# Kernel optimization log

Hardware: AMD Instinct MI355X
Metric: run time of the kernel (lower is better)

The kernel has to match this reference:

```python
import jax, jax.numpy as jnp
import numpy as np

NEG_SLOPE = 0.2  # PyG GATConv default
EPS = 1e-16      # PyG softmax denominator guard


def setup_inputs() -> dict:
    key = jax.random.key(0)
    k1, k2, k3, k4, k5 = jax.random.split(key, 5)
    N, E, D_in, H, C = 100000, 1600000, 128, 4, 32
    x = jax.random.normal(k1, (N, D_in), dtype=jnp.float32)
    edge_index = jax.random.randint(k2, (2, E), 0, N, dtype=jnp.int64)
    W = jax.random.normal(k3, (D_in, H * C), dtype=jnp.float32) * 0.05
    att_src = jax.random.normal(k4, (H, C), dtype=jnp.float32) * 0.05
    att_dst = jax.random.normal(k5, (H, C), dtype=jnp.float32) * 0.05
    bias = jnp.zeros((H * C,), dtype=jnp.float32)
    return {"x": x, "edge_index": edge_index, "W": W,
            "att_src": att_src, "att_dst": att_dst, "bias": bias}


def reference(x, edge_index, W, att_src, att_dst, bias):
    N = x.shape[0]
    H, C = att_src.shape
    # add self-loops (PyG default add_self_loops=True)
    loop = jnp.arange(N, dtype=edge_index.dtype)
    src = jnp.concatenate([edge_index[0], loop])  # [E+N]
    dst = jnp.concatenate([edge_index[1], loop])  # [E+N]

    # linear projection per head: [N, H, C]
    h = (x @ W).reshape(N, H, C)
    # per-node attention logits: [N, H]
    a_src = jnp.einsum('nhc,hc->nh', h, att_src)
    a_dst = jnp.einsum('nhc,hc->nh', h, att_dst)

    # per-edge logits with LeakyReLU: [E+N, H]
    e = jax.nn.leaky_relu(a_src[src] + a_dst[dst], NEG_SLOPE)

    # segment softmax over incoming edges of each dst node
    m = jax.ops.segment_max(e, dst, num_segments=N)          # [N, H]
    m = jnp.where(jnp.isfinite(m), m, 0.0)                    # empty segments
    ex = jnp.exp(e - m[dst])                                  # [E+N, H]
    s = jax.ops.segment_sum(ex, dst, num_segments=N)          # [N, H]
    alpha = ex / (s[dst] + EPS)                               # [E+N, H]

    # weighted message aggregation: [N, H, C]
    msgs = h[src] * alpha[:, :, None]
    out = jax.ops.segment_sum(msgs, dst, num_segments=N)

    # concat heads (attention_concat=True) + bias
    return out.reshape(N, H * C) + bias
```

## Files before the change

kernel.cpp:

```cpp
#include <hip/hip_runtime.h>

#define HC 128
#define NHEAD 4
#define HDIM 32
#define NEG 0.2f
#define GEPS 1e-16f
#define BSH 9
#define TILE 4096

__device__ __forceinline__ unsigned int bf16rn(float f) {
  unsigned int u = __float_as_uint(f);
  return (u + 0x7fffu + ((u >> 16) & 1u)) >> 16;
}

__global__ __launch_bounds__(256) void k_proj(const float* __restrict__ x,
                                              const float* __restrict__ W,
                                              const float* __restrict__ att_src,
                                              const float* __restrict__ att_dst,
                                              unsigned int* __restrict__ hb,
                                              float2* __restrict__ easrc,
                                              float2* __restrict__ eadst,
                                              int* __restrict__ bcnt, int N) {
  __shared__ float xs[64][129];
  if (blockIdx.x == 0) bcnt[threadIdx.x] = 0;
  int row0 = blockIdx.x * 64;
  for (int i = threadIdx.x; i < 2048; i += 256) {
    int r = i >> 5;
    int cc = (i & 31) << 2;
    float4 v = make_float4(0.f, 0.f, 0.f, 0.f);
    int row = row0 + r;
    if (row < N) v = *(const float4*)(x + (size_t)row * HC + cc);
    xs[r][cc + 0] = v.x;
    xs[r][cc + 1] = v.y;
    xs[r][cc + 2] = v.z;
    xs[r][cc + 3] = v.w;
  }
  __syncthreads();
  const int tr = (threadIdx.x >> 4) << 2;
  const int c0 = (threadIdx.x & 15) << 3;
  float acc[4][8];
#pragma unroll
  for (int i = 0; i < 4; ++i)
#pragma unroll
    for (int j = 0; j < 8; ++j) acc[i][j] = 0.f;

  for (int k = 0; k < 128; ++k) {
    const float4 w0 = *(const float4*)(W + k * HC + c0);
    const float4 w1 = *(const float4*)(W + k * HC + c0 + 4);
    float wv[8] = {w0.x, w0.y, w0.z, w0.w, w1.x, w1.y, w1.z, w1.w};
    float xv[4] = {xs[tr][k], xs[tr + 1][k], xs[tr + 2][k], xs[tr + 3][k]};
#pragma unroll
    for (int i = 0; i < 4; ++i)
#pragma unroll
      for (int j = 0; j < 8; ++j) acc[i][j] += xv[i] * wv[j];
  }
#pragma unroll
  for (int i = 0; i < 4; ++i) {
    int row = row0 + tr + i;
    if (row < N) {
      uint4 p;
      p.x = bf16rn(acc[i][0]) | (bf16rn(acc[i][1]) << 16);
      p.y = bf16rn(acc[i][2]) | (bf16rn(acc[i][3]) << 16);
      p.z = bf16rn(acc[i][4]) | (bf16rn(acc[i][5]) << 16);
      p.w = bf16rn(acc[i][6]) | (bf16rn(acc[i][7]) << 16);
      *(uint4*)(hb + (size_t)row * 64 + (c0 >> 1)) = p;
    }
  }
  int head = (threadIdx.x & 15) >> 2;
  int cc = c0 & 31;
  const float4 s0 = *(const float4*)(att_src + head * HDIM + cc);
  const float4 s1 = *(const float4*)(att_src + head * HDIM + cc + 4);
  const float4 d0 = *(const float4*)(att_dst + head * HDIM + cc);
  const float4 d1 = *(const float4*)(att_dst + head * HDIM + cc + 4);
  float asv[4], adv[4];
#pragma unroll
  for (int i = 0; i < 4; ++i) {
    asv[i] = acc[i][0] * s0.x + acc[i][1] * s0.y + acc[i][2] * s0.z + acc[i][3] * s0.w +
             acc[i][4] * s1.x + acc[i][5] * s1.y + acc[i][6] * s1.z + acc[i][7] * s1.w;
    adv[i] = acc[i][0] * d0.x + acc[i][1] * d0.y + acc[i][2] * d0.z + acc[i][3] * d0.w +
             acc[i][4] * d1.x + acc[i][5] * d1.y + acc[i][6] * d1.z + acc[i][7] * d1.w;
  }
#pragma unroll
  for (int off = 1; off < 4; off <<= 1) {
#pragma unroll
    for (int i = 0; i < 4; ++i) {
      asv[i] += __shfl_xor(asv[i], off);
      adv[i] += __shfl_xor(adv[i], off);
    }
  }
  if ((threadIdx.x & 3) == 0) {
#pragma unroll
    for (int i = 0; i < 4; ++i) {
      int row = row0 + tr + i;
      if (row < N) {
        easrc[row * NHEAD + head] = make_float2(__expf(asv[i]), __expf(NEG * asv[i]));
        eadst[row * NHEAD + head] = make_float2(__expf(adv[i]), __expf(NEG * adv[i]));
      }
    }
  }
}

__global__ __launch_bounds__(256) void k_bcount(const int* __restrict__ dst,
                                                int* __restrict__ bcnt, int E) {
  __shared__ int hist[256];
  int t = threadIdx.x;
  hist[t] = 0;
  __syncthreads();
  for (int e = blockIdx.x * 256 + t; e < E; e += gridDim.x * 256)
    atomicAdd(&hist[dst[e] >> BSH], 1);
  __syncthreads();
  if (hist[t]) atomicAdd(&bcnt[t], hist[t]);
}

__global__ __launch_bounds__(256) void k_bscan(const int* __restrict__ bcnt,
                                               int* __restrict__ bbase,
                                               int* __restrict__ bcur,
                                               int* __restrict__ rowptr,
                                               int* __restrict__ srcidx,
                                               int nbuck, int N, int E) {
  __shared__ int ss[256];
  int t = threadIdx.x;
  int v = (t < nbuck) ? bcnt[t] : 0;
  int x = v;
  ss[t] = x;
  __syncthreads();
  for (int off = 1; off < 256; off <<= 1) {
    int y = (t >= off) ? ss[t - off] : 0;
    __syncthreads();
    x += y;
    ss[t] = x;
    __syncthreads();
  }
  if (t < nbuck) {
    bbase[t] = x - v;
    bcur[t] = x - v;
  }
  if (t < 16) srcidx[E + t] = 0;
  if (t == 0) {
    bbase[nbuck] = E;
    rowptr[N] = E;
  }
}

__global__ __launch_bounds__(256) void k_partA(const int* __restrict__ src,
                                               const int* __restrict__ dst,
                                               int* __restrict__ bcur,
                                               unsigned int* __restrict__ ebuf,
                                               int E, int nbuck) {
  __shared__ unsigned int stage[TILE];
  __shared__ unsigned char bkt[TILE];
  __shared__ int hist[256], loff[256], lcur[256], gbase[256], ss[256];
  int t = threadIdx.x;
  int e0 = blockIdx.x * TILE;
  int cnt = min(TILE, E - e0);
  hist[t] = 0;
  __syncthreads();
  for (int i = t; i < cnt; i += 256)
    atomicAdd(&hist[dst[e0 + i] >> BSH], 1);
  __syncthreads();
  int v = hist[t];
  int x = v;
  ss[t] = x;
  __syncthreads();
  for (int off = 1; off < 256; off <<= 1) {
    int y = (t >= off) ? ss[t - off] : 0;
    __syncthreads();
    x += y;
    ss[t] = x;
    __syncthreads();
  }
  loff[t] = x - v;
  lcur[t] = x - v;
  __syncthreads();
  for (int i = t; i < cnt; i += 256) {
    int d = dst[e0 + i];
    int s = src[e0 + i];
    int b = d >> BSH;
    int r = atomicAdd(&lcur[b], 1);
    stage[r] = ((unsigned int)s << BSH) | (unsigned int)(d & ((1 << BSH) - 1));
    bkt[r] = (unsigned char)b;
  }
  __syncthreads();
  if (t < nbuck) {
    int c = lcur[t] - loff[t];
    gbase[t] = c ? atomicAdd(&bcur[t], c) : 0;
  }
  __syncthreads();
  for (int i = t; i < cnt; i += 256) {
    int b = bkt[i];
    ebuf[gbase[b] + (i - loff[b])] = stage[i];
  }
}

__global__ __launch_bounds__(512) void k_partB(const unsigned int* __restrict__ ebuf,
                                               const int* __restrict__ bbase,
                                               int* __restrict__ rowptr,
                                               int* __restrict__ srcidx, int N) {
  __shared__ int lcnt[512], ss[512];
  int b = blockIdx.x;
  int t = threadIdx.x;
  int beg = bbase[b], end = bbase[b + 1];
  lcnt[t] = 0;
  __syncthreads();
  for (int j = beg + t; j < end; j += 512)
    atomicAdd(&lcnt[ebuf[j] & 511], 1);
  __syncthreads();
  int v = lcnt[t];
  int x = v;
  ss[t] = x;
  __syncthreads();
  for (int off = 1; off < 512; off <<= 1) {
    int y = (t >= off) ? ss[t - off] : 0;
    __syncthreads();
    x += y;
    ss[t] = x;
    __syncthreads();
  }
  int ex = x - v;
  int node = (b << BSH) + t;
  if (node < N) rowptr[node] = beg + ex;
  __syncthreads();
  lcnt[t] = ex;
  __syncthreads();
  for (int j = beg + t; j < end; j += 512) {
    unsigned int v2 = ebuf[j];
    int pos = beg + atomicAdd(&lcnt[v2 & 511], 1);
    srcidx[pos] = (int)((v2 >> BSH) << 8);
  }
}

#define CONSUME(uu, ff)                                          \
  {                                                              \
    float ex = fmaxf((ff).x * edx, (ff).y * edy);                \
    accx = fmaf(__uint_as_float((uu) << 16), ex, accx);          \
    accy = fmaf(__uint_as_float((uu) & 0xffff0000u), ex, accy);  \
    ssum += ex;                                                  \
  }

__global__ __launch_bounds__(256) void k_agg(const int* __restrict__ rowptr,
                                             const int* __restrict__ srcoff,
                                             const unsigned int* __restrict__ hb,
                                             const float2* __restrict__ easrc,
                                             const float2* __restrict__ eadst,
                                             const float* __restrict__ bias,
                                             float* __restrict__ out, int N) {
  int n = blockIdx.x * 4 + (threadIdx.x >> 6);
  if (n >= N) return;
  int lane = threadIdx.x & 63;
  int head = lane >> 4;
  const char* hbp = (const char*)hb + (lane << 2);
  const char* eap = (const char*)easrc + (head << 3);
  float2 ed = eadst[n * NHEAD + head];
  float edx = ed.x, edy = ed.y;
  float2 es_own = *(const float2*)(eap + ((size_t)n << 5));
  float exs = fmaxf(es_own.x * edx, es_own.y * edy);
  unsigned int u = *(const unsigned*)(hbp + ((size_t)n << 8));
  float accx = __uint_as_float(u << 16) * exs;
  float accy = __uint_as_float(u & 0xffff0000u) * exs;
  float ssum = exs;

  int beg = rowptr[n], end = rowptr[n + 1];
  int rem = end - beg;
  int quads = rem >> 2;
  const int* sp = srcoff + beg;
  if (quads) {
    int a0 = sp[0], a1 = sp[1], a2 = sp[2], a3 = sp[3];
    int b0 = sp[4], b1 = sp[5], b2 = sp[6], b3 = sp[7];
    unsigned u0 = *(const unsigned*)(hbp + a0);
    unsigned u1 = *(const unsigned*)(hbp + a1);
    unsigned u2 = *(const unsigned*)(hbp + a2);
    unsigned u3 = *(const unsigned*)(hbp + a3);
    float2 f0 = *(const float2*)(eap + (a0 >> 3));
    float2 f1 = *(const float2*)(eap + (a1 >> 3));
    float2 f2 = *(const float2*)(eap + (a2 >> 3));
    float2 f3 = *(const float2*)(eap + (a3 >> 3));
    while (quads > 1) {
      int c0 = sp[8], c1 = sp[9], c2 = sp[10], c3 = sp[11];
      sp += 4;
      unsigned nu0 = *(const unsigned*)(hbp + b0);
      unsigned nu1 = *(const unsigned*)(hbp + b1);
      unsigned nu2 = *(const unsigned*)(hbp + b2);
      unsigned nu3 = *(const unsigned*)(hbp + b3);
      float2 nf0 = *(const float2*)(eap + (b0 >> 3));
      float2 nf1 = *(const float2*)(eap + (b1 >> 3));
      float2 nf2 = *(const float2*)(eap + (b2 >> 3));
      float2 nf3 = *(const float2*)(eap + (b3 >> 3));
      CONSUME(u0, f0) CONSUME(u1, f1) CONSUME(u2, f2) CONSUME(u3, f3)
      u0 = nu0; u1 = nu1; u2 = nu2; u3 = nu3;
      f0 = nf0; f1 = nf1; f2 = nf2; f3 = nf3;
      b0 = c0; b1 = c1; b2 = c2; b3 = c3;
      --quads;
    }
    CONSUME(u0, f0) CONSUME(u1, f1) CONSUME(u2, f2) CONSUME(u3, f3)
    sp += 4;
  }
  int tail = rem & 3;
  while (tail-- > 0) {
    int o = *sp++;
    unsigned uu = *(const unsigned*)(hbp + o);
    float2 ff = *(const float2*)(eap + (o >> 3));
    CONSUME(uu, ff)
  }
  float inv = 1.0f / (ssum + GEPS);
  float2 bv = *(const float2*)(bias + lane * 2);
  *(float2*)(out + (size_t)n * HC + lane * 2) =
      make_float2(fmaf(accx, inv, bv.x), fmaf(accy, inv, bv.y));
}

extern "C" void kernel_launch(void* const* d_in, const int* in_sizes, int n_in,
                              void* d_out, int out_size, void* d_ws, size_t ws_size,
                              hipStream_t stream) {
  const float* x       = (const float*)d_in[0];
  const int*   ei      = (const int*)d_in[1];
  const float* W       = (const float*)d_in[2];
  const float* att_src = (const float*)d_in[3];
  const float* att_dst = (const float*)d_in[4];
  const float* bias    = (const float*)d_in[5];
  float* out = (float*)d_out;

  const int N = in_sizes[0] / HC;
  const int E = in_sizes[1] / 2;
  const int* src = ei;
  const int* dst = ei + E;
  const int nbuck = (N + (1 << BSH) - 1) >> BSH;

  unsigned int* hb = (unsigned int*)d_ws;
  float2* easrc = (float2*)(hb + (size_t)N * 64);
  float2* eadst = easrc + (size_t)N * NHEAD;
  int* rowptr = (int*)(eadst + (size_t)N * NHEAD);
  int* srcidx = rowptr + (N + 1);
  unsigned int* ebuf = (unsigned int*)(srcidx + E + 16);
  int* bcnt = (int*)(ebuf + E);
  int* bbase = bcnt + 256;
  int* bcur = bbase + 257;

  k_proj<<<(N + 63) / 64, 256, 0, stream>>>(x, W, att_src, att_dst, hb, easrc, eadst, bcnt, N);
  k_bcount<<<1024, 256, 0, stream>>>(dst, bcnt, E);
  k_bscan<<<1, 256, 0, stream>>>(bcnt, bbase, bcur, rowptr, srcidx, nbuck, N, E);
  k_partA<<<(E + TILE - 1) / TILE, 256, 0, stream>>>(src, dst, bcur, ebuf, E, nbuck);
  k_partB<<<nbuck, 512, 0, stream>>>(ebuf, bbase, rowptr, srcidx, N);
  k_agg<<<(N + 3) / 4, 256, 0, stream>>>(rowptr, srcidx, hb, easrc, eadst, bias, out, N);
}
```

Measured before the change: 333.3 us.

## Aggregate with 32 lanes per node using 8-byte gathers and deeper prefetch

The aggregation kernel now gives each destination node 32 lanes instead of 64. Each lane loads a uint2 holding four bf16 features and keeps four accumulators, so each 64-wide wave covers two nodes. The gather loop is restructured into two ping-pong quad buffers (A/B) so more gathers are in flight, and the final store becomes a float4. This halves the per-edge index and logit loads per node and raises memory-level parallelism, at the cost of more registers and divergence when two nodes in the same wave have different degrees.

Measured after the change: 328.5 us. No clear change (-1.4%).

```diff
diff --git a/kernel.cpp b/kernel.cpp
--- a/kernel.cpp
+++ b/kernel.cpp
@@ -229,13 +229,24 @@
   }
 }
 
-#define CONSUME(uu, ff)                                          \
-  {                                                              \
-    float ex = fmaxf((ff).x * edx, (ff).y * edy);                \
-    accx = fmaf(__uint_as_float((uu) << 16), ex, accx);          \
-    accy = fmaf(__uint_as_float((uu) & 0xffff0000u), ex, accy);  \
-    ssum += ex;                                                  \
-  }
+#define CONS(uu, ff)                                               \
+  {                                                                \
+    float ex = fmaxf((ff).x * edx, (ff).y * edy);                  \
+    acc0 = fmaf(__uint_as_float((uu).x << 16), ex, acc0);          \
+    acc1 = fmaf(__uint_as_float((uu).x & 0xffff0000u), ex, acc1);  \
+    acc2 = fmaf(__uint_as_float((uu).y << 16), ex, acc2);          \
+    acc3 = fmaf(__uint_as_float((uu).y & 0xffff0000u), ex, acc3);  \
+    ssum += ex;                                                    \
+  }
+#define GATHER(U, F, O)                                            \
+  U##0 = *(const uint2*)(hbp + O##0);                              \
+  U##1 = *(const uint2*)(hbp + O##1);                              \
+  U##2 = *(const uint2*)(hbp + O##2);                              \
+  U##3 = *(const uint2*)(hbp + O##3);                              \
+  F##0 = *(const float2*)(eap + (O##0 >> 3));                      \
+  F##1 = *(const float2*)(eap + (O##1 >> 3));                      \
+  F##2 = *(const float2*)(eap + (O##2 >> 3));                      \
+  F##3 = *(const float2*)(eap + (O##3 >> 3));
 
 __global__ __launch_bounds__(256) void k_agg(const int* __restrict__ rowptr,
                                              const int* __restrict__ srcoff,
@@ -244,67 +255,59 @@
                                              const float2* __restrict__ eadst,
                                              const float* __restrict__ bias,
                                              float* __restrict__ out, int N) {
-  int n = blockIdx.x * 4 + (threadIdx.x >> 6);
+  int n = blockIdx.x * 8 + (threadIdx.x >> 5);
   if (n >= N) return;
-  int lane = threadIdx.x & 63;
-  int head = lane >> 4;
-  const char* hbp = (const char*)hb + (lane << 2);
+  int lane = threadIdx.x & 31;
+  int head = lane >> 3;
+  const char* hbp = (const char*)hb + (lane << 3);
   const char* eap = (const char*)easrc + (head << 3);
   float2 ed = eadst[n * NHEAD + head];
   float edx = ed.x, edy = ed.y;
   float2 es_own = *(const float2*)(eap + ((size_t)n << 5));
   float exs = fmaxf(es_own.x * edx, es_own.y * edy);
-  unsigned int u = *(const unsigned*)(hbp + ((size_t)n << 8));
-  float accx = __uint_as_float(u << 16) * exs;
-  float accy = __uint_as_float(u & 0xffff0000u) * exs;
+  uint2 us = *(const uint2*)(hbp + ((size_t)n << 8));
+  float acc0 = __uint_as_float(us.x << 16) * exs;
+  float acc1 = __uint_as_float(us.x & 0xffff0000u) * exs;
+  float acc2 = __uint_as_float(us.y << 16) * exs;
+  float acc3 = __uint_as_float(us.y & 0xffff0000u) * exs;
   float ssum = exs;
 
   int beg = rowptr[n], end = rowptr[n + 1];
   int rem = end - beg;
-  int quads = rem >> 2;
+  int Q = rem >> 2;
   const int* sp = srcoff + beg;
-  if (quads) {
-    int a0 = sp[0], a1 = sp[1], a2 = sp[2], a3 = sp[3];
-    int b0 = sp[4], b1 = sp[5], b2 = sp[6], b3 = sp[7];
-    unsigned u0 = *(const unsigned*)(hbp + a0);
-    unsigned u1 = *(const unsigned*)(hbp + a1);
-    unsigned u2 = *(const unsigned*)(hbp + a2);
-    unsigned u3 = *(const unsigned*)(hbp + a3);
-    float2 f0 = *(const float2*)(eap + (a0 >> 3));
-    float2 f1 = *(const float2*)(eap + (a1 >> 3));
-    float2 f2 = *(const float2*)(eap + (a2 >> 3));
-    float2 f3 = *(const float2*)(eap + (a3 >> 3));
-    while (quads > 1) {
-      int c0 = sp[8], c1 = sp[9], c2 = sp[10], c3 = sp[11];
-      sp += 4;
-      unsigned nu0 = *(const unsigned*)(hbp + b0);
-      unsigned nu1 = *(const unsigned*)(hbp + b1);
-      unsigned nu2 = *(const unsigned*)(hbp + b2);
-      unsigned nu3 = *(const unsigned*)(hbp + b3);
-      float2 nf0 = *(const float2*)(eap + (b0 >> 3));
-      float2 nf1 = *(const float2*)(eap + (b1 >> 3));
-      float2 nf2 = *(const float2*)(eap + (b2 >> 3));
-      float2 nf3 = *(const float2*)(eap + (b3 >> 3));
-      CONSUME(u0, f0) CONSUME(u1, f1) CONSUME(u2, f2) CONSUME(u3, f3)
-      u0 = nu0; u1 = nu1; u2 = nu2; u3 = nu3;
-      f0 = nf0; f1 = nf1; f2 = nf2; f3 = nf3;
-      b0 = c0; b1 = c1; b2 = c2; b3 = c3;
-      --quads;
+  if (Q) {
+    int oA0 = sp[0], oA1 = sp[1], oA2 = sp[2], oA3 = sp[3];
+    int oB0 = 0, oB1 = 0, oB2 = 0, oB3 = 0;
+    uint2 uA0, uA1, uA2, uA3, uB0, uB1, uB2, uB3;
+    float2 fA0, fA1, fA2, fA3, fB0, fB1, fB2, fB3;
+    GATHER(uA, fA, oA)
+    if (Q >= 2) { oB0 = sp[4]; oB1 = sp[5]; oB2 = sp[6]; oB3 = sp[7]; }
+    while (Q >= 2) {
+      GATHER(uB, fB, oB)
+      oA0 = sp[8]; oA1 = sp[9]; oA2 = sp[10]; oA3 = sp[11];
+      CONS(uA0, fA0) CONS(uA1, fA1) CONS(uA2, fA2) CONS(uA3, fA3)
+      GATHER(uA, fA, oA)
+      oB0 = sp[12]; oB1 = sp[13]; oB2 = sp[14]; oB3 = sp[15];
+      CONS(uB0, fB0) CONS(uB1, fB1) CONS(uB2, fB2) CONS(uB3, fB3)
+      sp += 8;
+      Q -= 2;
     }
-    CONSUME(u0, f0) CONSUME(u1, f1) CONSUME(u2, f2) CONSUME(u3, f3)
-    sp += 4;
+    if (Q == 1) { CONS(uA0, fA0) CONS(uA1, fA1) CONS(uA2, fA2) CONS(uA3, fA3) }
   }
   int tail = rem & 3;
+  const int* tp = srcoff + beg + (rem & ~3);
   while (tail-- > 0) {
-    int o = *sp++;
-    unsigned uu = *(const unsigned*)(hbp + o);
+    int o = *tp++;
+    uint2 uu = *(const uint2*)(hbp + o);
     float2 ff = *(const float2*)(eap + (o >> 3));
-    CONSUME(uu, ff)
+    CONS(uu, ff)
   }
   float inv = 1.0f / (ssum + GEPS);
-  float2 bv = *(const float2*)(bias + lane * 2);
-  *(float2*)(out + (size_t)n * HC + lane * 2) =
-      make_float2(fmaf(accx, inv, bv.x), fmaf(accy, inv, bv.y));
+  const float4 bv = *(const float4*)(bias + lane * 4);
+  *(float4*)(out + (size_t)n * HC + lane * 4) =
+      make_float4(fmaf(acc0, inv, bv.x), fmaf(acc1, inv, bv.y),
+                  fmaf(acc2, inv, bv.z), fmaf(acc3, inv, bv.w));
 }
 
 extern "C" void kernel_launch(void* const* d_in, const int* in_sizes, int n_in,
@@ -339,5 +342,5 @@
   k_bscan<<<1, 256, 0, stream>>>(bcnt, bbase, bcur, rowptr, srcidx, nbuck, N, E);
   k_partA<<<(E + TILE - 1) / TILE, 256, 0, stream>>>(src, dst, bcur, ebuf, E, nbuck);
   k_partB<<<nbuck, 512, 0, stream>>>(ebuf, bbase, rowptr, srcidx, N);
-  k_agg<<<(N + 3) / 4, 256, 0, stream>>>(rowptr, srcidx, hb, easrc, eadst, bias, out, N);
-}
+  k_agg<<<(N + 7) / 8, 256, 0, stream>>>(rowptr, srcidx, hb, easrc, eadst, bias, out, N);
+}
```
